# Optimization experiments

Measured on AMD Instinct MI355X. Metric: run time of the kernel, lower is better.

The kernel has to match this reference:

```python
import jax, jax.numpy as jnp
from jax import lax
import numpy as np

B, C, T = 8, 512, 8192
RATIO = 2
K = 12  # filter taps for both up and down FIR


def kaiser_sinc_filter1d(cutoff, half_width, kernel_size):
    # Faithful port of BigVGAN's kaiser_sinc_filter1d (even kernel_size path)
    half_size = kernel_size // 2
    delta_f = 4.0 * half_width
    A = 2.285 * (half_size - 1) * np.pi * delta_f + 7.95
    if A > 50.0:
        beta = 0.1102 * (A - 8.7)
    elif A >= 21.0:
        beta = 0.5842 * (A - 21.0) ** 0.4 + 0.07886 * (A - 21.0)
    else:
        beta = 0.0
    window = np.kaiser(kernel_size, beta)
    time = np.arange(-half_size, half_size) + 0.5  # even kernel
    filt = 2.0 * cutoff * window * np.sinc(2.0 * cutoff * time)
    filt = filt / filt.sum()
    return jnp.asarray(filt, dtype=jnp.float32)


def setup_inputs() -> dict:
    key = jax.random.key(0)
    k1, k2 = jax.random.split(key)
    x = jax.random.normal(k1, (B, C, T), dtype=jnp.float32)
    # Snake per-channel alpha parameter in LOG scale (alpha_logscale=True)
    alpha = 0.1 * jax.random.normal(k2, (C,), dtype=jnp.float32)
    # Fixed anti-aliasing low-pass filters (buffers)
    up_filter = kaiser_sinc_filter1d(cutoff=0.5 / RATIO, half_width=0.6 / RATIO, kernel_size=K)
    down_filter = kaiser_sinc_filter1d(cutoff=0.5 / RATIO, half_width=0.6 / RATIO, kernel_size=K)
    return {"x": x, "alpha": alpha, "up_filter": up_filter, "down_filter": down_filter}


def _forward(x, alpha, up_filter, down_filter):
    Bc, Cc, Tc = x.shape
    dn = ("NCH", "OIH", "NCH")
    # ---- UpSample1d: replicate-pad, grouped conv_transpose (stride=RATIO), crop ----
    pad = K // RATIO - 1                                  # 5
    pad_left = pad * RATIO + (K - RATIO) // 2             # 15
    pad_right = pad * RATIO + (K - RATIO + 1) // 2        # 15
    xp = jnp.pad(x, ((0, 0), (0, 0), (pad, pad)), mode="edge")
    w_up = jnp.broadcast_to(up_filter[None, None, :], (Cc, 1, K))
    # conv_transpose1d(stride=s) == input-dilated conv with flipped kernel, full padding
    y = RATIO * lax.conv_general_dilated(
        xp, jnp.flip(w_up, axis=-1),
        window_strides=(1,), padding=[(K - 1, K - 1)],
        lhs_dilation=(RATIO,), dimension_numbers=dn,
        feature_group_count=Cc)
    y = y[..., pad_left:-pad_right]                       # [B, C, RATIO*T]
    # ---- Snake activation (logscale alpha) ----
    a = jnp.exp(alpha)[None, :, None]
    y = y + (1.0 / (a + 1e-9)) * jnp.square(jnp.sin(a * y))
    # ---- DownSample1d: replicate-pad, grouped strided FIR conv ----
    dpl = K // 2 - 1                                       # 5 (even kernel)
    dpr = K // 2                                           # 6
    yp = jnp.pad(y, ((0, 0), (0, 0), (dpl, dpr)), mode="edge")
    w_dn = jnp.broadcast_to(down_filter[None, None, :], (Cc, 1, K))
    out = lax.conv_general_dilated(
        yp, w_dn,
        window_strides=(RATIO,), padding=[(0, 0)],
        dimension_numbers=dn, feature_group_count=Cc)
    return out                                             # [B, C, T]


def reference(x, alpha, up_filter, down_filter):
    return _forward(x, alpha, up_filter, down_filter)
```

## Files before the change

kernel.cpp:

```cpp
#include <hip/hip_runtime.h>

#define T_LEN 8192
#define C_N   512
#define BLOCK 256
#define NCHUNK 4
#define INV_2PI 0.15915494309189535f


__global__ __launch_bounds__(BLOCK) void act1d_fused(
    const float* __restrict__ x,
    const float* __restrict__ alpha,
    const float* __restrict__ wup_g,
    const float* __restrict__ wdn_g,
    float* __restrict__ out)
{
    const int bx    = blockIdx.x;
    const int chunk = bx & (NCHUNK - 1);
    const int bc    = bx >> 2;
    const int c     = bc & (C_N - 1);
    const int tid   = threadIdx.x;
    const int lane  = tid & 63;
    const int N     = chunk * 2048 + 8 * tid;

    const float* __restrict__ xrow = x   + (size_t)bc * T_LEN;
    float*       __restrict__ orow = out + (size_t)bc * T_LEN;

    float u2[12], wdn[12];
#pragma unroll
    for (int i = 0; i < 12; ++i) {
        u2[i]  = wup_g[i] + wup_g[i];
        wdn[i] = wdn_g[i];
    }
    const float a     = __expf(alpha[c]);
    const float inv_a = 1.0f / (a + 1e-9f);
    const float ka    = a * INV_2PI;

    float xr[16];
    if (N >= 8) {
        const float4 A = *reinterpret_cast<const float4*>(xrow + N - 8);
        const float4 Bv = *reinterpret_cast<const float4*>(xrow + N - 4);
        const float4 Cv = *reinterpret_cast<const float4*>(xrow + N);
        const float4 Dv = *reinterpret_cast<const float4*>(xrow + N + 4);
        xr[0]=A.x; xr[1]=A.y; xr[2]=A.z; xr[3]=A.w;
        xr[4]=Bv.x; xr[5]=Bv.y; xr[6]=Bv.z; xr[7]=Bv.w;
        xr[8]=Cv.x; xr[9]=Cv.y; xr[10]=Cv.z; xr[11]=Cv.w;
        xr[12]=Dv.x; xr[13]=Dv.y; xr[14]=Dv.z; xr[15]=Dv.w;
    } else {
#pragma unroll
        for (int u = 0; u < 16; ++u)
            xr[u] = xrow[max(N - 8 + u, 0)];
    }

    float yv[16];
#pragma unroll
    for (int p = 0; p < 8; ++p) {
        float ae = 0.0f, ao = 0.0f;
#pragma unroll
        for (int t = 0; t < 6; ++t) {
            ae = fmaf(u2[2 * t + 1], xr[7 + p - t], ae);
            ao = fmaf(u2[2 * t],     xr[8 + p - t], ao);
        }
        yv[2 * p]     = ae;
        yv[2 * p + 1] = ao;
    }
#pragma unroll
    for (int q = 0; q < 16; ++q) {
        const float s = __builtin_amdgcn_sinf(ka * yv[q]);
        yv[q] = fmaf(s * s, inv_a, yv[q]);
    }

    if (N == 0) {
        yv[1] = yv[2] = yv[3] = yv[4] = yv[5] = yv[6];
    }

    float h[11];
#pragma unroll
    for (int v = 0; v < 11; ++v)
        h[v] = __shfl_down(yv[v], 1, 64);

    if (lane == 63) {
        float xh[6];
        if (N + 13 < T_LEN) {
            const float4 A = *reinterpret_cast<const float4*>(xrow + N + 8);
            const float4 Bv = *reinterpret_cast<const float4*>(xrow + N + 12);
            xh[0]=A.x; xh[1]=A.y; xh[2]=A.z; xh[3]=A.w; xh[4]=Bv.x; xh[5]=Bv.y;
        } else {
#pragma unroll
            for (int u = 0; u < 6; ++u)
                xh[u] = xrow[min(N + 8 + u, T_LEN - 1)];
        }
#define XX(u) ((u) < 16 ? xr[(u) < 16 ? (u) : 0] : xh[(u) >= 16 ? (u) - 16 : 0])
#pragma unroll
        for (int pp = 0; pp < 6; ++pp) {
            float ae = 0.0f;
#pragma unroll
            for (int t = 0; t < 6; ++t)
                ae = fmaf(u2[2 * t + 1], XX(15 + pp - t), ae);
            {
                const float s = __builtin_amdgcn_sinf(ka * ae);
                ae = fmaf(s * s, inv_a, ae);
            }
            h[2 * pp] = ae;
            if (pp < 5) {
                float ao = 0.0f;
#pragma unroll
                for (int t = 0; t < 6; ++t)
                    ao = fmaf(u2[2 * t], XX(16 + pp - t), ao);
                const float s = __builtin_amdgcn_sinf(ka * ao);
                ao = fmaf(s * s, inv_a, ao);
                h[2 * pp + 1] = ao;
            }
        }
#undef XX
    }

    if (N == T_LEN - 8) {
        h[6] = h[7] = h[8] = h[9] = h[10] = h[5];
    }

    float o[8];
#pragma unroll
    for (int r = 0; r < 8; ++r) {
        float acc = 0.0f;
#pragma unroll
        for (int k = 0; k < 12; ++k) {
            const int j = 2 * r + k;
            acc = fmaf(wdn[k], (j < 15 ? yv[j + 1] : h[j - 15]), acc);
        }
        o[r] = acc;
    }

    *reinterpret_cast<float4*>(orow + N)     = make_float4(o[0], o[1], o[2], o[3]);
    *reinterpret_cast<float4*>(orow + N + 4) = make_float4(o[4], o[5], o[6], o[7]);
}

extern "C" void kernel_launch(void* const* d_in, const int* in_sizes, int n_in,
                              void* d_out, int out_size, void* d_ws, size_t ws_size,
                              hipStream_t stream)
{
    const float* x     = (const float*)d_in[0];
    const float* alpha = (const float*)d_in[1];
    const float* wup   = (const float*)d_in[2];
    const float* wdn   = (const float*)d_in[3];
    float*       out   = (float*)d_out;

    const int B_N  = out_size / (C_N * T_LEN);
    const int grid = B_N * C_N * NCHUNK;

    act1d_fused<<<grid, BLOCK, 0, stream>>>(x, alpha, wup, wdn, out);
}
```

Baseline: 56.14 us.

## Process two row segments per block with early loads and nontemporal stores

Halves the grid so each block handles two 2048-sample chunks of a row, issuing both input loads before any compute to increase memory-level parallelism. Filter and alpha setup is amortized over two segments, and outputs use nontemporal stores to avoid polluting cache. This raises register pressure per thread and may reduce occupancy.

```diff
diff --git a/kernel.cpp b/kernel.cpp
--- a/kernel.cpp
+++ b/kernel.cpp
@@ -3,54 +3,38 @@
 #define T_LEN 8192
 #define C_N   512
 #define BLOCK 256
-#define NCHUNK 4
+#define OPT   8
+#define TCHUNK (BLOCK * OPT)
 #define INV_2PI 0.15915494309189535f
 
+typedef float f32x4 __attribute__((ext_vector_type(4)));
 
-__global__ __launch_bounds__(BLOCK) void act1d_fused(
-    const float* __restrict__ x,
-    const float* __restrict__ alpha,
-    const float* __restrict__ wup_g,
-    const float* __restrict__ wdn_g,
-    float* __restrict__ out)
+
+__device__ __forceinline__ void load_xr(const float* __restrict__ xrow,
+                                        int N, float xr[16])
 {
-    const int bx    = blockIdx.x;
-    const int chunk = bx & (NCHUNK - 1);
-    const int bc    = bx >> 2;
-    const int c     = bc & (C_N - 1);
-    const int tid   = threadIdx.x;
-    const int lane  = tid & 63;
-    const int N     = chunk * 2048 + 8 * tid;
-
-    const float* __restrict__ xrow = x   + (size_t)bc * T_LEN;
-    float*       __restrict__ orow = out + (size_t)bc * T_LEN;
-
-    float u2[12], wdn[12];
+    if (N >= 8) {
 #pragma unroll
-    for (int i = 0; i < 12; ++i) {
-        u2[i]  = wup_g[i] + wup_g[i];
-        wdn[i] = wdn_g[i];
-    }
-    const float a     = __expf(alpha[c]);
-    const float inv_a = 1.0f / (a + 1e-9f);
-    const float ka    = a * INV_2PI;
-
-    float xr[16];
-    if (N >= 8) {
-        const float4 A = *reinterpret_cast<const float4*>(xrow + N - 8);
-        const float4 Bv = *reinterpret_cast<const float4*>(xrow + N - 4);
-        const float4 Cv = *reinterpret_cast<const float4*>(xrow + N);
-        const float4 Dv = *reinterpret_cast<const float4*>(xrow + N + 4);
-        xr[0]=A.x; xr[1]=A.y; xr[2]=A.z; xr[3]=A.w;
-        xr[4]=Bv.x; xr[5]=Bv.y; xr[6]=Bv.z; xr[7]=Bv.w;
-        xr[8]=Cv.x; xr[9]=Cv.y; xr[10]=Cv.z; xr[11]=Cv.w;
-        xr[12]=Dv.x; xr[13]=Dv.y; xr[14]=Dv.z; xr[15]=Dv.w;
+        for (int w = 0; w < 4; ++w) {
+            const float4 t4 = *reinterpret_cast<const float4*>(xrow + N - 8 + 4 * w);
+            xr[4 * w + 0] = t4.x;
+            xr[4 * w + 1] = t4.y;
+            xr[4 * w + 2] = t4.z;
+            xr[4 * w + 3] = t4.w;
+        }
     } else {
 #pragma unroll
         for (int u = 0; u < 16; ++u)
             xr[u] = xrow[max(N - 8 + u, 0)];
     }
+}
 
+__device__ __forceinline__ void compute_segment(
+    const float xr[16], int N, int lane,
+    const float* __restrict__ xrow, float* __restrict__ orow,
+    const float u2[12], const float wdn[12],
+    float inv_a, float ka)
+{
     float yv[16];
 #pragma unroll
     for (int p = 0; p < 8; ++p) {
@@ -114,13 +98,13 @@
 #undef XX
     }
 
-    if (N == T_LEN - 8) {
+    if (N == T_LEN - OPT) {
         h[6] = h[7] = h[8] = h[9] = h[10] = h[5];
     }
 
-    float o[8];
+    float o[OPT];
 #pragma unroll
-    for (int r = 0; r < 8; ++r) {
+    for (int r = 0; r < OPT; ++r) {
         float acc = 0.0f;
 #pragma unroll
         for (int k = 0; k < 12; ++k) {
@@ -130,8 +114,48 @@
         o[r] = acc;
     }
 
-    *reinterpret_cast<float4*>(orow + N)     = make_float4(o[0], o[1], o[2], o[3]);
-    *reinterpret_cast<float4*>(orow + N + 4) = make_float4(o[4], o[5], o[6], o[7]);
+    f32x4 s0 = { o[0], o[1], o[2], o[3] };
+    f32x4 s1 = { o[4], o[5], o[6], o[7] };
+    __builtin_nontemporal_store(s0, reinterpret_cast<f32x4*>(orow + N));
+    __builtin_nontemporal_store(s1, reinterpret_cast<f32x4*>(orow + N + 4));
+}
+
+__global__ __launch_bounds__(BLOCK) void act1d_fused(
+    const float* __restrict__ x,
+    const float* __restrict__ alpha,
+    const float* __restrict__ wup_g,
+    const float* __restrict__ wdn_g,
+    float* __restrict__ out)
+{
+    const int bx   = blockIdx.x;
+    const int p    = bx & 1;
+    const int bc   = bx >> 1;
+    const int c    = bc & (C_N - 1);
+    const int tid  = threadIdx.x;
+    const int lane = tid & 63;
+
+    const int NA = p * TCHUNK + OPT * tid;
+    const int NB = (p + 2) * TCHUNK + OPT * tid;
+
+    const float* __restrict__ xrow = x   + (size_t)bc * T_LEN;
+    float*       __restrict__ orow = out + (size_t)bc * T_LEN;
+
+    float xrA[16], xrB[16];
+    load_xr(xrow, NA, xrA);
+    load_xr(xrow, NB, xrB);
+
+    float u2[12], wdn[12];
+#pragma unroll
+    for (int i = 0; i < 12; ++i) {
+        u2[i]  = wup_g[i] + wup_g[i];
+        wdn[i] = wdn_g[i];
+    }
+    const float a     = __expf(alpha[c]);
+    const float inv_a = 1.0f / (a + 1e-9f);
+    const float ka    = a * INV_2PI;
+
+    compute_segment(xrA, NA, lane, xrow, orow, u2, wdn, inv_a, ka);
+    compute_segment(xrB, NB, lane, xrow, orow, u2, wdn, inv_a, ka);
 }
 
 extern "C" void kernel_launch(void* const* d_in, const int* in_sizes, int n_in,
@@ -145,7 +169,7 @@
     float*       out   = (float*)d_out;
 
     const int B_N  = out_size / (C_N * T_LEN);
-    const int grid = B_N * C_N * NCHUNK;
+    const int grid = B_N * C_N * 2;
 
     act1d_fused<<<grid, BLOCK, 0, stream>>>(x, alpha, wup, wdn, out);
 }
```

Measured after the change: 55.88 us. About the same (-0.5%).
